# Performance work log

Measured on AMD Instinct MI355X. Metric: run time of the kernel, lower is better.

## Reference

```python
import jax, jax.numpy as jnp
import numpy as np

B, T, N, C = 4, 6, 512, 8
HID, FEAT, EMB, IN_DIM = 64, 16, 32, 1
KS, KC, HORIZON = 3, 2, 3
ALPHA = 3.0

def _init(key, shape):
    fin = shape[-2] if len(shape) >= 2 else shape[-1]
    return jax.random.normal(key, shape, dtype=jnp.float32) * (1.0 / fin) ** 0.5

def setup_inputs():
    ks = jax.random.split(jax.random.key(0), 32)
    L_enc = (IN_DIM + FEAT + HID) * KS * KC
    L_dec = (HID + FEAT + HID) * KS * KC
    return {
        "X_seq": jax.random.normal(ks[0], (B, T, N, C), dtype=jnp.float32),
        "As": jax.random.uniform(ks[1], (N, N), dtype=jnp.float32) / N,
        "Ac": jax.random.uniform(ks[2], (C, C), dtype=jnp.float32) / C,
        "feature": jax.random.normal(ks[3], (N, FEAT), dtype=jnp.float32),
        "Wu_S": _init(ks[4], (C, HID)), "Wv_S": _init(ks[5], (C, HID)),
        "Wu_C": _init(ks[6], (N, HID)), "Wv_C": _init(ks[7], (N, HID)),
        "mfS_w1": _init(ks[8], (4, 2, 256)), "mfS_b1": jnp.zeros((4, 256), jnp.float32),
        "mfS_w2": _init(ks[9], (4, 256, 256)), "mfS_b2": jnp.zeros((4, 256), jnp.float32),
        "mfC_w1": _init(ks[10], (4, 2, 256)), "mfC_b1": jnp.zeros((4, 256), jnp.float32),
        "mfC_w2": _init(ks[11], (4, 256, 256)), "mfC_b2": jnp.zeros((4, 256), jnp.float32),
        "enc_gW": _init(ks[12], (L_enc, 2 * HID)), "enc_gb": jnp.zeros((2 * HID,), jnp.float32),
        "enc_cW": _init(ks[13], (L_enc, HID)), "enc_cb": jnp.zeros((HID,), jnp.float32),
        "dec_gW": _init(ks[14], (L_dec, 2 * HID)), "dec_gb": jnp.zeros((2 * HID,), jnp.float32),
        "dec_cW": _init(ks[15], (L_dec, HID)), "dec_cb": jnp.zeros((HID,), jnp.float32),
        "out_w1": _init(ks[16], (HID, EMB)), "out_b1": jnp.zeros((EMB,), jnp.float32),
        "out_w2": _init(ks[17], (EMB, IN_DIM)), "out_b2": jnp.zeros((IN_DIM,), jnp.float32),
    }

def _mlp(x, w1, b1, w2, b2):
    return jax.nn.relu(x @ w1 + b1) @ w2 + b2

def _mixed_fusion(A, P, w1, b1, w2, b2):
    # node_feat = [rowsum(A), rowsum(P)]; key/value MLPs indexed 0:key_A 1:key_P 2:val_A 3:val_P
    nf = jnp.stack([A.sum(-1), P.sum(-1)], axis=-1)            # [n, 2]
    An, Pn = A @ nf, P @ nf
    key = _mlp(An, w1[0], b1[0], w2[0], b2[0]) + _mlp(Pn, w1[1], b1[1], w2[1], b2[1])
    val = _mlp(An, w1[2], b1[2], w2[2], b2[2]) + _mlp(Pn, w1[3], b1[3], w2[3], b2[3])
    a = jax.nn.sigmoid(key @ val.T)
    return a * A + (1.0 - a) * P

def _adaptive_graph(Xf, Wu, Wv):
    U = jnp.tanh(ALPHA * Xf @ Wu)                              # [b,t,n,h]
    V = jnp.tanh(ALPHA * Xf @ Wv)
    M = jnp.einsum('btnh,btmh->nm', U, V)
    # Ps = softmax(relu(M - M^T)) matches einsum pair in torch source
    return jax.nn.softmax(jax.nn.relu(M - M.T), axis=-1)

def _cheby(G, K):
    mats = [jnp.eye(G.shape[0], dtype=G.dtype), G]
    for _ in range(2, K):
        mats.append(2.0 * G @ mats[-1] - mats[-2])
    return jnp.stack(mats[:K], axis=0)                         # [K, n, n]

def _bdg(X, Gs_set, Gc_set, W, b):
    # X: [b,n,c,l]; fused Ks x Kc Chebyshev mode products; cat order (k, j, l) matches torch cat
    t1 = jnp.einsum('bncl,knm->kbmcl', X, Gs_set)
    t2 = jnp.einsum('kbmcl,jcd->bmdkjl', t1, Gc_set)
    feat = t2.reshape(t2.shape[0], t2.shape[1], t2.shape[2], -1)
    return feat @ W + b

def _cell(Xt, Ht, featx, Gs_set, Gc_set, gW, gb, cW, cb):
    XH = jnp.concatenate([Xt, Ht, featx], axis=-1)
    uv = _bdg(XH, Gs_set, Gc_set, gW, gb)
    update = jax.nn.sigmoid(uv[..., :HID])
    reset = jax.nn.sigmoid(uv[..., HID:])
    cand_in = jnp.concatenate([Xt, reset * Ht, featx], axis=-1)
    cand = jnp.tanh(_bdg(cand_in, Gs_set, Gc_set, cW, cb))
    return (1.0 - update) * Ht + update * cand

def _forward(X_seq, As, Ac, feature, Wu_S, Wv_S, Wu_C, Wv_C,
             mfS_w1, mfS_b1, mfS_w2, mfS_b2, mfC_w1, mfC_b1, mfC_w2, mfC_b2,
             enc_gW, enc_gb, enc_cW, enc_cb, dec_gW, dec_gb, dec_cW, dec_cb,
             out_w1, out_b1, out_w2, out_b2):
    # MGP_Gen: adaptive spatial / categorical graphs fused with priors
    Ps = _adaptive_graph(X_seq, Wu_S, Wv_S)
    Gs = _mixed_fusion(As, Ps, mfS_w1, mfS_b1, mfS_w2, mfS_b2)
    Xc = jnp.swapaxes(X_seq, 2, 3)                             # [b,t,c,n]
    Pc = _adaptive_graph(Xc, Wu_C, Wv_C)
    Gc = _mixed_fusion(Ac, Pc, mfC_w1, mfC_b1, mfC_w2, mfC_b2)
    Gs_set, Gc_set = _cheby(Gs, KS), _cheby(Gc, KC)
    featx = jnp.broadcast_to(feature[None, :, None, :], (B, N, C, FEAT))
    X5 = X_seq[..., None]                                      # [b,t,n,c,1]
    Ht = jnp.zeros((B, N, C, HID), dtype=X_seq.dtype)
    for t in range(T):                                         # encoder GRU over history
        Ht = _cell(X5[:, t], Ht, featx, Gs_set, Gc_set, enc_gW, enc_gb, enc_cW, enc_cb)
    deco_in, Hd = Ht, Ht
    outs = []
    for _ in range(HORIZON):
        Hd = _cell(deco_in, Hd, featx, Gs_set, Gc_set, dec_gW, dec_gb, dec_cW, dec_cb)
        outs.append(_mlp(Hd, out_w1, out_b1, out_w2, out_b2))
        deco_in = Hd
    return jnp.stack(outs, axis=1)                             # [b, horizon, n, c, 1]

def reference(X_seq, As, Ac, feature, Wu_S, Wv_S, Wu_C, Wv_C, mfS_w1, mfS_b1, mfS_w2, mfS_b2, mfC_w1, mfC_b1, mfC_w2, mfC_b2, enc_gW, enc_gb, enc_cW, enc_cb, dec_gW, dec_gb, dec_cW, dec_cb, out_w1, out_b1, out_w2, out_b2):
    return _forward(X_seq, As, Ac, feature, Wu_S, Wv_S, Wu_C, Wv_C, mfS_w1, mfS_b1, mfS_w2, mfS_b2, mfC_w1, mfC_b1, mfC_w2, mfC_b2, enc_gW, enc_gb, enc_cW, enc_cb, dec_gW, dec_gb, dec_cW, dec_cb, out_w1, out_b1, out_w2, out_b2)
```

## Files before the change

### kernel.cpp

```cpp
#include <hip/hip_runtime.h>
#include <math.h>

constexpr int kB = 4, kT = 6, kN = 512, kC = 8;
constexpr int kH = 64, kF = 16, kE = 32;
constexpr int kKS = 3, kKC = 2, kHOR = 3;
constexpr int kBT = kB * kT;
constexpr int kRK = kBT * kH;
constexpr int L_ENC = 1 + kH + kF;
constexpr int L_DEC = kH + kH + kF;
constexpr int PL_ENC = 96;
constexpr int PL_DEC = 160;
constexpr int KP_ENC = 3 * PL_ENC;
constexpr int KP_DGF = 288;
constexpr int KP_DEC = 3 * PL_DEC;
constexpr float kALPHA = 3.0f;

typedef unsigned short ushortT;
typedef short short8 __attribute__((ext_vector_type(8)));
typedef float f32x4 __attribute__((ext_vector_type(4)));

__device__ __forceinline__ float sigm(float x) { return 1.0f / (1.0f + __expf(-x)); }

__device__ __forceinline__ ushortT f2bf(float f) {
    union { float f; unsigned int u; } v; v.f = f;
    unsigned int r = v.u + 0x7fffu + ((v.u >> 16) & 1u);
    return (ushortT)(r >> 16);
}

__device__ __forceinline__ void fma44(const float4& a, const float4& b, float acc[4][4]) {
    acc[0][0] += a.x*b.x; acc[0][1] += a.x*b.y; acc[0][2] += a.x*b.z; acc[0][3] += a.x*b.w;
    acc[1][0] += a.y*b.x; acc[1][1] += a.y*b.y; acc[1][2] += a.y*b.z; acc[1][3] += a.y*b.w;
    acc[2][0] += a.z*b.x; acc[2][1] += a.z*b.y; acc[2][2] += a.z*b.z; acc[2][3] += a.z*b.w;
    acc[3][0] += a.w*b.x; acc[3][1] += a.w*b.y; acc[3][2] += a.w*b.z; acc[3][3] += a.w*b.w;
}


__global__ __launch_bounds__(256) void k_uvproj_s(
    const float* __restrict__ X, const float* __restrict__ Wu, const float* __restrict__ Wv,
    float* __restrict__ Upr, float* __restrict__ Vpr)
{
    int idx = blockIdx.x * blockDim.x + threadIdx.x;
    if (idx >= kN * kBT * kH) return;
    int h = idx % kH; int bt = (idx / kH) % kBT; int n = idx / (kH * kBT);
    const float* xr = X + ((size_t)bt * kN + n) * kC;
    float u = 0.f, v = 0.f;
#pragma unroll
    for (int c = 0; c < kC; ++c) { float x = xr[c]; u += x * Wu[c*kH + h]; v += x * Wv[c*kH + h]; }
    Upr[(size_t)n * kRK + bt * kH + h] = tanhf(kALPHA * u);
    Vpr[(size_t)n * kRK + bt * kH + h] = tanhf(kALPHA * v);
}

__global__ __launch_bounds__(512) void k_uvproj_c2(
    const float* __restrict__ X, const float* __restrict__ WuC, const float* __restrict__ WvC,
    float* __restrict__ Uc, float* __restrict__ Vc)
{
    __shared__ float Xs[4096];
    __shared__ float Wus[4096], Wvs[4096];
    int bt = blockIdx.x, tid = threadIdx.x;
    for (int i = tid; i < 4096; i += 512) Xs[i] = X[(size_t)bt*4096 + i];
    int c = tid >> 6, h = tid & 63;
    float u = 0.f, v = 0.f;
    for (int n0 = 0; n0 < 512; n0 += 64) {
        __syncthreads();
        for (int i = tid; i < 4096; i += 512) { Wus[i] = WuC[n0*64 + i]; Wvs[i] = WvC[n0*64 + i]; }
        __syncthreads();
#pragma unroll 8
        for (int nn = 0; nn < 64; ++nn) {
            float x = Xs[(n0+nn)*8 + c];
            u += x * Wus[nn*64 + h];
            v += x * Wvs[nn*64 + h];
        }
    }
    Uc[(size_t)bt*512 + c*64 + h] = tanhf(kALPHA * u);
    Vc[(size_t)bt*512 + c*64 + h] = tanhf(kALPHA * v);
}

__global__ __launch_bounds__(512) void k_mc2(
    const float* __restrict__ Uc, const float* __restrict__ Vc, float* __restrict__ Mc)
{
    __shared__ float red[512];
    int tid = threadIdx.x;
    int cd = tid & 63, kc = tid >> 6;
    int c = cd >> 3, d = cd & 7;
    float s = 0.f;
    for (int q = kc*192; q < kc*192 + 192; ++q) {
        int bt = q >> 6, h = q & 63;
        s += Uc[(size_t)bt*512 + c*64 + h] * Vc[(size_t)bt*512 + d*64 + h];
    }
    red[tid] = s; __syncthreads();
    for (int st = 256; st >= 64; st >>= 1) { if (tid < st) red[tid] += red[tid + st]; __syncthreads(); }
    if (tid < 64) Mc[tid] = red[tid];
}

__global__ __launch_bounds__(256) void k_nfa(const float* __restrict__ A, float* __restrict__ nf)
{
    int i = blockIdx.x, tid = threadIdx.x;
    __shared__ float sa[256];
    float a = 0.f;
    for (int j = tid; j < kN; j += 256) a += A[(size_t)i*kN + j];
    sa[tid] = a; __syncthreads();
    for (int s = 128; s > 0; s >>= 1) { if (tid < s) sa[tid] += sa[tid+s]; __syncthreads(); }
    if (!tid) { nf[i*2] = sa[0]; nf[i*2+1] = 1.0f; }
}

__global__ __launch_bounds__(256) void k_softmax_anpn(
    const float* __restrict__ M, const float* __restrict__ A, const float* __restrict__ nf,
    float* __restrict__ P, float* __restrict__ An, float* __restrict__ Pn)
{
    int i = blockIdx.x, tid = threadIdx.x;
    __shared__ float s0[256], s1[256], s2[256], s3[256], s4[256];
    float mx = -1e30f;
    for (int j = tid; j < kN; j += 256)
        mx = fmaxf(mx, fmaxf(M[(size_t)i*kN + j] - M[(size_t)j*kN + i], 0.f));
    s0[tid] = mx; __syncthreads();
    for (int s = 128; s > 0; s >>= 1) { if (tid < s) s0[tid] = fmaxf(s0[tid], s0[tid+s]); __syncthreads(); }
    mx = s0[0]; __syncthreads();
    float sum=0, pn0=0, pn1=0, an0=0, an1=0;
    for (int j = tid; j < kN; j += 256) {
        float v = fmaxf(M[(size_t)i*kN + j] - M[(size_t)j*kN + i], 0.f);
        float e = __expf(v - mx);
        P[(size_t)i*kN + j] = e;
        float n0 = nf[2*j], n1 = nf[2*j+1];
        float a = A[(size_t)i*kN + j];
        sum += e; pn0 += e*n0; pn1 += e*n1; an0 += a*n0; an1 += a*n1;
    }
    s0[tid]=sum; s1[tid]=pn0; s2[tid]=pn1; s3[tid]=an0; s4[tid]=an1; __syncthreads();
    for (int s = 128; s > 0; s >>= 1) {
        if (tid < s) { s0[tid]+=s0[tid+s]; s1[tid]+=s1[tid+s]; s2[tid]+=s2[tid+s]; s3[tid]+=s3[tid+s]; s4[tid]+=s4[tid+s]; }
        __syncthreads();
    }
    float inv = 1.f / s0[0];
    if (!tid) { Pn[i*2] = s1[0]*inv; Pn[i*2+1] = s2[0]*inv; An[i*2] = s3[0]; An[i*2+1] = s4[0]; }
    __syncthreads();
    for (int j = tid; j < kN; j += 256) P[(size_t)i*kN + j] *= inv;
}

__global__ __launch_bounds__(256) void k_mlp1cat(
    const float* __restrict__ An, const float* __restrict__ Pn,
    const float* __restrict__ w1, const float* __restrict__ b1, int ia, int ip,
    float* __restrict__ hidAP)
{
    int idx = blockIdx.x * 256 + threadIdx.x;
    if (idx >= 512 * 512) return;
    int col = idx & 511, i = idx >> 9;
    float v;
    if (col < 256) {
        const float* w = w1 + (size_t)ia * 512; const float* b = b1 + (size_t)ia * 256;
        v = An[i*2]*w[col] + An[i*2+1]*w[256 + col] + b[col];
    } else {
        int o = col - 256;
        const float* w = w1 + (size_t)ip * 512; const float* b = b1 + (size_t)ip * 256;
        v = Pn[i*2]*w[o] + Pn[i*2+1]*w[256 + o] + b[o];
    }
    hidAP[idx] = fmaxf(v, 0.f);
}

__global__ __launch_bounds__(256) void k_prep_w2t(
    const float* __restrict__ w2, float* __restrict__ w2tK, float* __restrict__ w2tV)
{
    int idx = blockIdx.x * 256 + threadIdx.x;
    if (idx >= 256 * 512) return;
    int kk = idx & 511, n = idx >> 9;
    int j = kk >> 8, k = kk & 255;
    w2tK[idx] = w2[(size_t)(0 + j)*65536 + k*256 + n];
    w2tV[idx] = w2[(size_t)(2 + j)*65536 + k*256 + n];
}

__global__ __launch_bounds__(256) void k_gemm_ntsk(
    const float* __restrict__ A, const float* __restrict__ B, float* __restrict__ part,
    int M, int N, int K, int skl)
{
    __shared__ __align__(16) float sA[32][68];
    __shared__ __align__(16) float sB[32][68];
    int tid = threadIdx.x, tx = tid & 15, ty = tid >> 4;
    int j0 = blockIdx.x * 64, i0 = blockIdx.y * 64;
    int kb = blockIdx.z * skl;
    float acc[4][4] = {};
    for (int k0 = kb; k0 < kb + skl; k0 += 32) {
#pragma unroll
        for (int it = 0; it < 2; ++it) {
            int q = tid + it * 256;
            int row = q >> 3, ks = (q & 7) * 4;
            float4 va = *(const float4*)&A[(size_t)(i0 + row)*K + k0 + ks];
            float4 vb = *(const float4*)&B[(size_t)(j0 + row)*K + k0 + ks];
            sA[ks+0][row] = va.x; sA[ks+1][row] = va.y; sA[ks+2][row] = va.z; sA[ks+3][row] = va.w;
            sB[ks+0][row] = vb.x; sB[ks+1][row] = vb.y; sB[ks+2][row] = vb.z; sB[ks+3][row] = vb.w;
        }
        __syncthreads();
#pragma unroll
        for (int kk = 0; kk < 32; ++kk) {
            float4 a = *(const float4*)&sA[kk][ty*4];
            float4 b = *(const float4*)&sB[kk][tx*4];
            fma44(a, b, acc);
        }
        __syncthreads();
    }
    float* dst = part + (size_t)blockIdx.z * M * N;
#pragma unroll
    for (int i = 0; i < 4; ++i)
#pragma unroll
        for (int j = 0; j < 4; ++j)
            dst[(size_t)(i0 + ty*4 + i)*N + j0 + tx*4 + j] = acc[i][j];
}

__global__ __launch_bounds__(256) void k_redep(
    const float* __restrict__ part, int SK, int total, int N,
    float* __restrict__ C, int mode,
    const float* __restrict__ p1, const float* __restrict__ p2)
{
    int idx = blockIdx.x * 256 + threadIdx.x;
    if (idx >= total) return;
    float s = 0.f;
    for (int k = 0; k < SK; ++k) s += part[(size_t)k*total + idx];
    if (mode == 1) { float a = sigm(s); s = a*p1[idx] + (1.f - a)*p2[idx]; }
    else if (mode == 2) { int col = idx % N; s += p1[col] + p2[col]; }
    C[idx] = s;
}

__global__ __launch_bounds__(256) void k_catmlp2(
    const float* __restrict__ Mc, const float* __restrict__ Ac,
    const float* __restrict__ w1, const float* __restrict__ b1,
    const float* __restrict__ w2, const float* __restrict__ b2,
    float* __restrict__ keyval)
{
    __shared__ float Pcs[64], rsA[8], Ans[16], Pns[16];
    __shared__ float hA[8][256], hP[8][256];
    int tid = threadIdx.x;
    int kv = blockIdx.x, c0 = blockIdx.y * 64;
    int qa = kv*2, qp = kv*2 + 1;
    if (tid < 8) {
        int i = tid;
        float row[8]; float mx = -1e30f;
#pragma unroll
        for (int j = 0; j < 8; ++j) { float v = fmaxf(Mc[i*8+j] - Mc[j*8+i], 0.f); row[j] = v; mx = fmaxf(mx, v); }
        float s = 0.f;
#pragma unroll
        for (int j = 0; j < 8; ++j) { row[j] = __expf(row[j] - mx); s += row[j]; }
        float inv = 1.f / s;
#pragma unroll
        for (int j = 0; j < 8; ++j) Pcs[i*8+j] = row[j] * inv;
        float a = 0.f;
#pragma unroll
        for (int j = 0; j < 8; ++j) a += Ac[i*8+j];
        rsA[i] = a;
    }
    __syncthreads();
    if (tid < 16) {
        int i = tid >> 1, comp = tid & 1;
        float an = 0.f, pn = 0.f;
#pragma unroll
        for (int j = 0; j < 8; ++j) {
            float nfj = comp ? 1.f : rsA[j];
            an += Ac[i*8+j] * nfj; pn += Pcs[i*8+j] * nfj;
        }
        Ans[i*2+comp] = an; Pns[i*2+comp] = pn;
    }
    __syncthreads();
    for (int e = tid; e < 2048; e += 256) {
        int i = e >> 8, o = e & 255;
        hA[i][o] = fmaxf(Ans[i*2]*w1[qa*512 + o] + Ans[i*2+1]*w1[qa*512 + 256 + o] + b1[qa*256 + o], 0.f);
        hP[i][o] = fmaxf(Pns[i*2]*w1[qp*512 + o] + Pns[i*2+1]*w1[qp*512 + 256 + o] + b1[qp*256 + o], 0.f);
    }
    __syncthreads();
    for (int e = tid; e < 512; e += 256) {
        int i = e >> 6, oc = c0 + (e & 63);
        float s = b2[qa*256 + oc] + b2[qp*256 + oc];
        for (int k = 0; k < 256; ++k)
            s += hA[i][k]*w2[(size_t)qa*65536 + k*256 + oc] + hP[i][k]*w2[(size_t)qp*65536 + k*256 + oc];
        keyval[(size_t)kv*2048 + i*256 + oc] = s;
    }
}

__global__ void k_gcfuse2(const float* __restrict__ keyval, const float* __restrict__ Mc,
                          const float* __restrict__ Ac, float* __restrict__ GcF)
{
    __shared__ float Pcs[64];
    int t = threadIdx.x; if (t >= 64) return;
    if (t < 8) {
        int i = t;
        float row[8]; float mx = -1e30f;
#pragma unroll
        for (int j = 0; j < 8; ++j) { float v = fmaxf(Mc[i*8+j] - Mc[j*8+i], 0.f); row[j] = v; mx = fmaxf(mx, v); }
        float s = 0.f;
#pragma unroll
        for (int j = 0; j < 8; ++j) { row[j] = __expf(row[j] - mx); s += row[j]; }
        float inv = 1.f / s;
#pragma unroll
        for (int j = 0; j < 8; ++j) Pcs[i*8+j] = row[j] * inv;
    }
    __syncthreads();
    int c = t >> 3, d = t & 7;
    const float* key = keyval;
    const float* val = keyval + 2048;
    float s = 0.f;
    for (int k = 0; k < 256; ++k) s += key[c*256 + k] * val[d*256 + k];
    float a = sigm(s);
    GcF[c*8 + d] = a*Ac[c*8 + d] + (1.f - a)*Pcs[c*8 + d];
}


__global__ void k_transp(const float* __restrict__ G, ushortT* __restrict__ Gt)
{
    __shared__ float tile[32][33];
    int bx = blockIdx.x * 32, by = blockIdx.y * 32;
    int x = threadIdx.x, y0 = threadIdx.y;
    for (int yy = y0; yy < 32; yy += 8) tile[yy][x] = G[(size_t)(by+yy)*kN + bx + x];
    __syncthreads();
    for (int yy = y0; yy < 32; yy += 8) Gt[(size_t)(bx+yy)*kN + by + x] = f2bf(tile[x][yy]);
}

__global__ __launch_bounds__(256) void k_prep_wt(
    const float* __restrict__ W, ushortT* __restrict__ WT,
    int L, int PL, int KP, int outW, int mode)
{
    int idx = blockIdx.x * blockDim.x + threadIdx.x;
    if (idx >= 2 * outW * KP) return;
    int qp = idx % KP, o = idx / KP;
    int kk = qp / PL, l = qp - kk * PL;
    int lo;
    if (mode == 1) lo = (l < 64) ? l + 1 : (l == 64) ? 0 : (l < 80) ? L : (l - 15);
    else lo = l;
    int j = o / outW, oo = o - j * outW;
    float v = (lo < L) ? W[(size_t)((kk*2 + j)*L + lo) * outW + oo] : 0.f;
    WT[idx] = f2bf(v);
}

__global__ __launch_bounds__(256) void k_prep_wtgd(
    const float* __restrict__ W, ushortT* __restrict__ WT)
{
    int idx = blockIdx.x * blockDim.x + threadIdx.x;
    if (idx >= 256 * KP_DGF) return;
    int qp = idx % KP_DGF, o = idx / KP_DGF;
    int k = qp / 96, p = qp - k * 96;
    int j = o >> 7, oo = o & 127;
    int base = (k*2 + j) * L_DEC;
    float v;
    if (p < 64)      v = W[(size_t)(base + p)*128 + oo] + W[(size_t)(base + 64 + p)*128 + oo];
    else if (p < 80) v = W[(size_t)(base + 128 + (p - 64))*128 + oo];
    else             v = 0.f;
    WT[idx] = f2bf(v);
}

__global__ __launch_bounds__(256) void k_cheby_mfma(
    const ushortT* __restrict__ Gst, ushortT* __restrict__ Gst2)
{
    __shared__ short sA[128][40];
    __shared__ short sB[128][40];
    int tid = threadIdx.x;
    int m0 = blockIdx.y * 128, j0 = blockIdx.x * 128;
    int w = tid >> 6, lane = tid & 63, wr = w >> 1, wc = w & 1;
    f32x4 acc[4][4];
#pragma unroll
    for (int i = 0; i < 4; ++i)
#pragma unroll
        for (int j = 0; j < 4; ++j) acc[i][j] = (f32x4){0.f, 0.f, 0.f, 0.f};
    for (int k0 = 0; k0 < kN; k0 += 32) {
        {
            int row = tid >> 1, lc = (tid & 1) * 16;
            const ushortT* p = Gst + (size_t)(m0 + row)*kN + k0 + lc;
            *(short8*)&sA[row][lc]     = *(const short8*)p;
            *(short8*)&sA[row][lc + 8] = *(const short8*)(p + 8);
        }
        {
            int kr = tid & 31, jc = (tid >> 5) * 8;
#pragma unroll
            for (int rep = 0; rep < 2; ++rep) {
                short8 v = *(const short8*)(Gst + (size_t)(k0 + kr)*kN + j0 + jc + rep*64);
#pragma unroll
                for (int i = 0; i < 8; ++i) sB[jc + rep*64 + i][kr] = v[i];
            }
        }
        __syncthreads();
        short8 af[4], bfr[4];
#pragma unroll
        for (int mi = 0; mi < 4; ++mi)
            af[mi] = *(const short8*)&sA[wr*64 + mi*16 + (lane & 15)][(lane >> 4) * 8];
#pragma unroll
        for (int ni = 0; ni < 4; ++ni)
            bfr[ni] = *(const short8*)&sB[wc*64 + ni*16 + (lane & 15)][(lane >> 4) * 8];
#pragma unroll
        for (int mi = 0; mi < 4; ++mi)
#pragma unroll
            for (int ni = 0; ni < 4; ++ni)
                acc[mi][ni] = __builtin_amdgcn_mfma_f32_16x16x32_bf16(af[mi], bfr[ni], acc[mi][ni], 0, 0, 0);
        __syncthreads();
    }
#pragma unroll
    for (int mi = 0; mi < 4; ++mi) {
#pragma unroll
        for (int ni = 0; ni < 4; ++ni) {
            int row0 = m0 + wr*64 + mi*16 + (lane >> 4) * 4;
            int col  = j0 + wc*64 + ni*16 + (lane & 15);
#pragma unroll
            for (int q = 0; q < 4; ++q) {
                int row = row0 + q;
                Gst2[(size_t)row*kN + col] = f2bf(2.f*acc[mi][ni][q] - (row == col ? 1.f : 0.f));
            }
        }
    }
}

template<int CLP, int PL, int ACTW, int OFF>
__global__ __launch_bounds__(256) void k_t1m(
    const ushortT* __restrict__ Gst, const ushortT* __restrict__ Xin, ushortT* __restrict__ Yout)
{
    __shared__ short sA[128][40];
    __shared__ short sB[128][40];
    int tid = threadIdx.x;
    int ki = blockIdx.z >> 2, b = blockIdx.z & 3;
    const ushortT* A = Gst + (size_t)ki * kN * kN;
    const ushortT* B = Xin + (size_t)b * kN * CLP;
    ushortT* C = Yout + (size_t)(ki*4 + b) * kN * CLP;
    int m0 = blockIdx.y * 128, j0 = blockIdx.x * 128;
    int w = tid >> 6, lane = tid & 63, wr = w >> 1, wc = w & 1;
    int kr = tid & 31, jc = (tid >> 5) * 8;
    int colr0, colr1;
    { int j = j0 + jc;      int cg = j / ACTW; colr0 = cg*PL + OFF + (j - cg*ACTW); }
    { int j = j0 + jc + 64; int cg = j / ACTW; colr1 = cg*PL + OFF + (j - cg*ACTW); }
    f32x4 acc[4][4];
#pragma unroll
    for (int i = 0; i < 4; ++i)
#pragma unroll
        for (int j = 0; j < 4; ++j) acc[i][j] = (f32x4){0.f, 0.f, 0.f, 0.f};

    for (int k0 = 0; k0 < kN; k0 += 32) {
        {
            int row = tid >> 1, lc = (tid & 1) * 16;
            const ushortT* p = A + (size_t)(m0 + row)*kN + k0 + lc;
            *(short8*)&sA[row][lc]     = *(const short8*)p;
            *(short8*)&sA[row][lc + 8] = *(const short8*)(p + 8);
        }
        {
            short8 v0 = *(const short8*)(B + (size_t)(k0 + kr)*CLP + colr0);
            short8 v1 = *(const short8*)(B + (size_t)(k0 + kr)*CLP + colr1);
#pragma unroll
            for (int i = 0; i < 8; ++i) sB[jc + i][kr] = v0[i];
#pragma unroll
            for (int i = 0; i < 8; ++i) sB[jc + 64 + i][kr] = v1[i];
        }
        __syncthreads();
        short8 af[4], bfr[4];
#pragma unroll
        for (int mi = 0; mi < 4; ++mi)
            af[mi] = *(const short8*)&sA[wr*64 + mi*16 + (lane & 15)][(lane >> 4) * 8];
#pragma unroll
        for (int ni = 0; ni < 4; ++ni)
            bfr[ni] = *(const short8*)&sB[wc*64 + ni*16 + (lane & 15)][(lane >> 4) * 8];
#pragma unroll
        for (int mi = 0; mi < 4; ++mi)
#pragma unroll
            for (int ni = 0; ni < 4; ++ni)
                acc[mi][ni] = __builtin_amdgcn_mfma_f32_16x16x32_bf16(af[mi], bfr[ni], acc[mi][ni], 0, 0, 0);
        __syncthreads();
    }
#pragma unroll
    for (int mi = 0; mi < 4; ++mi) {
#pragma unroll
        for (int ni = 0; ni < 4; ++ni) {
            int row = m0 + wr*64 + mi*16 + (lane >> 4) * 4;
            int fj = j0 + wc*64 + ni*16;
            int cg = fj / ACTW;
            int col = cg*PL + OFF + (fj - cg*ACTW) + (lane & 15);
#pragma unroll
            for (int q = 0; q < 4; ++q)
                C[(size_t)(row + q)*CLP + col] = f2bf(acc[mi][ni][q]);
        }
    }
}

template<int PL, int NQ, int MODE, int FN>
__global__ __launch_bounds__(256) void k_gg(
    const ushortT* __restrict__ XH, const ushortT* __restrict__ Yb,
    const ushortT* __restrict__ WT, float* __restrict__ Cout)
{
    constexpr int BN = 32 * FN;
    constexpr int KP = NQ * 32;
    constexpr int Ntot = 64 * FN;
    __shared__ short sA[128][40];
    __shared__ short sB[BN][40];
    int tid = threadIdx.x;
    int r0 = blockIdx.y * 128, j0 = blockIdx.x * BN;
    int b = r0 >> 12, rr = r0 & 4095;
    const ushortT* src0 = XH + (size_t)r0 * PL;
    const ushortT* src1 = Yb + ((size_t)b       * 4096 + rr) * PL;
    const ushortT* src2 = Yb + ((size_t)(4 + b) * 4096 + rr) * PL;
    int w = tid >> 6, lane = tid & 63, wr = w >> 1, wc = w & 1;
    f32x4 acc[4][FN];
#pragma unroll
    for (int i = 0; i < 4; ++i)
#pragma unroll
        for (int j = 0; j < FN; ++j) acc[i][j] = (f32x4){0.f, 0.f, 0.f, 0.f};

    for (int q = 0; q < NQ; ++q) {
        int k, off;
        if (MODE == 0)      { k = q/3; off = (q - k*3)*32; }
        else if (MODE == 1) { k = q/3; int part = q - k*3; off = (part < 2) ? part*32 : 128; }
        else                { k = q/5; off = (q - k*5)*32; }
        const ushortT* Ap = (k == 0) ? src0 : (k == 1) ? src1 : src2;
        {
            int row = tid >> 1, lc = (tid & 1) * 16;
            const ushortT* p = Ap + (size_t)row * PL + off + lc;
            *(short8*)&sA[row][lc]     = *(const short8*)p;
            *(short8*)&sA[row][lc + 8] = *(const short8*)(p + 8);
        }
        if (FN == 4) {
            int col = tid >> 1, seg = (tid & 1) * 16;
            const ushortT* p = WT + (size_t)(j0 + col)*KP + q*32 + seg;
            *(short8*)&sB[col][seg]     = *(const short8*)p;
            *(short8*)&sB[col][seg + 8] = *(const short8*)(p + 8);
        } else {
            int col = tid >> 2, seg = (tid & 3) * 8;
            *(short8*)&sB[col][seg] = *(const short8*)(WT + (size_t)(j0 + col)*KP + q*32 + seg);
        }
        __syncthreads();
        short8 af[4], bfr[FN];
#pragma unroll
        for (int mi = 0; mi < 4; ++mi)
            af[mi] = *(const short8*)&sA[wr*64 + mi*16 + (lane & 15)][(lane >> 4) * 8];
#pragma unroll
        for (int ni = 0; ni < FN; ++ni)
            bfr[ni] = *(const short8*)&sB[wc*16*FN + ni*16 + (lane & 15)][(lane >> 4) * 8];
#pragma unroll
        for (int mi = 0; mi < 4; ++mi)
#pragma unroll
            for (int ni = 0; ni < FN; ++ni)
                acc[mi][ni] = __builtin_amdgcn_mfma_f32_16x16x32_bf16(af[mi], bfr[ni], acc[mi][ni], 0, 0, 0);
        __syncthreads();
    }
#pragma unroll
    for (int mi = 0; mi < 4; ++mi) {
#pragma unroll
        for (int ni = 0; ni < FN; ++ni) {
            int row = r0 + wr*64 + mi*16 + (lane >> 4) * 4;
            int col = j0 + wc*16*FN + ni*16 + (lane & 15);
#pragma unroll
            for (int q = 0; q < 4; ++q)
                Cout[(size_t)(row + q)*Ntot + col] = acc[mi][ni][q];
        }
    }
}


template<int PL, int XOFF>
__global__ __launch_bounds__(256) void k_gates_ep(
    const float* __restrict__ Gg, const float* __restrict__ GcM,
    const float* __restrict__ gb, const float* __restrict__ Ht,
    float* __restrict__ upd, ushortT* __restrict__ XH)
{
    __shared__ float sG[8][256];
    __shared__ float GcS[64];
    int tid = threadIdx.x, bm = blockIdx.x;
    const float* src = Gg + (size_t)bm * 2048;
    for (int i = tid; i < 2048; i += 256) sG[i >> 8][i & 255] = src[i];
    if (tid < 64) GcS[tid] = GcM[tid];
    __syncthreads();
    int d = tid >> 5, o0 = (tid & 31) * 4;
    size_t rb = (size_t)bm * 8 + d;
#pragma unroll
    for (int q = 0; q < 4; ++q) {
        int o = o0 + q;
        float pre = sG[d][o] + gb[o];
#pragma unroll
        for (int c = 0; c < 8; ++c) pre += GcS[c*8 + d] * sG[c][128 + o];
        float g = sigm(pre);
        if (o < kH) upd[rb*kH + o] = g;
        else {
            int h = o - kH;
            XH[rb*PL + XOFF + h] = f2bf(g * Ht[rb*kH + h]);
        }
    }
}

template<int MODE>
__global__ __launch_bounds__(256) void k_cand_ep(
    const float* __restrict__ Gc2, const float* __restrict__ GcM,
    const float* __restrict__ cb, const float* __restrict__ upd,
    float* __restrict__ Ht, ushortT* __restrict__ XHo,
    const float* __restrict__ X, int tnext,
    const float* __restrict__ ow1, const float* __restrict__ ob1,
    const float* __restrict__ ow2, const float* __restrict__ ob2,
    float* __restrict__ out, int hz)
{
    __shared__ float sG[8][128];
    __shared__ float GcS[64];
    __shared__ float Hn[8][65];
    __shared__ float Pp[8][32];
    int tid = threadIdx.x, bm = blockIdx.x;
    const float* src = Gc2 + (size_t)bm * 1024;
    for (int i = tid; i < 1024; i += 256) sG[i >> 7][i & 127] = src[i];
    if (tid < 64) GcS[tid] = GcM[tid];
    __syncthreads();
    int d = tid >> 5, o0 = (tid & 31) * 2;
    size_t rb = (size_t)bm * 8 + d;
#pragma unroll
    for (int jj = 0; jj < 2; ++jj) {
        int o = o0 + jj;
        float pre = sG[d][o] + cb[o];
#pragma unroll
        for (int c = 0; c < 8; ++c) pre += GcS[c*8 + d] * sG[c][64 + o];
        float cv = tanhf(pre);
        float u = upd[rb*kH + o];
        float h0 = Ht[rb*kH + o];
        float hn = (1.f - u)*h0 + u*cv;
        Ht[rb*kH + o] = hn;
        if (MODE >= 2) Hn[d][o] = hn;
        if (MODE == 0)      XHo[rb*PL_ENC + o] = f2bf(hn);
        else if (MODE <= 2) XHo[rb*PL_DEC + o] = f2bf(hn);
    }
    if (MODE == 0) {
        if (tid < 8) {
            int r = bm*8 + tid;
            int c2 = r & 7, m = (r >> 3) & 511, b2 = r >> 12;
            XHo[(size_t)r*PL_ENC + 64] = f2bf(X[(((size_t)b2*kT + tnext)*kN + m)*kC + c2]);
        }
    }
    if (MODE >= 2) {
        __syncthreads();
        int row = tid >> 5, e = tid & 31;
        float s = ob1[e];
#pragma unroll
        for (int k = 0; k < kH; ++k) s += Hn[row][k] * ow1[k*kE + e];
        Pp[row][e] = fmaxf(s, 0.f) * ow2[e];
        __syncthreads();
        if (tid < 8) {
            float v = ob2[0];
#pragma unroll
            for (int e2 = 0; e2 < 32; ++e2) v += Pp[tid][e2];
            int r = bm*8 + tid;
            int c2 = r & 7, m = (r >> 3) & 511, b2 = r >> 12;
            out[((size_t)(b2*kHOR + hz)*kN + m)*kC + c2] = v;
        }
    }
}

__global__ __launch_bounds__(256) void k_build_enc0(
    const float* __restrict__ X, const float* __restrict__ featr, ushortT* __restrict__ XH)
{
    int idx = blockIdx.x * blockDim.x + threadIdx.x;
    if (idx >= 16384 * PL_ENC) return;
    int l = idx % PL_ENC; int r = idx / PL_ENC;
    float v;
    if (l < 64)       v = 0.f;
    else if (l == 64) { int c = r & 7, m = (r >> 3) & 511, b = r >> 12; v = X[(((size_t)b*kT)*kN + m)*kC + c]; }
    else if (l < 80)  v = 0.f;
    else              { int m = (r >> 3) & 511; v = featr[m*kF + (l - 80)]; }
    XH[idx] = f2bf(v);
}

__global__ __launch_bounds__(256) void k_initdec(
    const float* __restrict__ featr, ushortT* __restrict__ XHd)
{
    int idx = blockIdx.x * blockDim.x + threadIdx.x;
    if (idx >= 16384 * 32) return;
    int l2 = idx & 31; int r = idx >> 5;
    float v = (l2 < 16) ? featr[((r >> 3) & 511)*kF + l2] : 0.f;
    XHd[(size_t)r*PL_DEC + 128 + l2] = f2bf(v);
}

extern "C" void kernel_launch(void* const* d_in, const int* in_sizes, int n_in,
                              void* d_out, int out_size, void* d_ws, size_t ws_size,
                              hipStream_t stream)
{
    (void)in_sizes; (void)n_in; (void)out_size; (void)ws_size;
    const float* X      = (const float*)d_in[0];
    const float* As     = (const float*)d_in[1];
    const float* Ac     = (const float*)d_in[2];
    const float* featr  = (const float*)d_in[3];
    const float* WuS    = (const float*)d_in[4];
    const float* WvS    = (const float*)d_in[5];
    const float* WuC    = (const float*)d_in[6];
    const float* WvC    = (const float*)d_in[7];
    const float* mfS_w1 = (const float*)d_in[8];
    const float* mfS_b1 = (const float*)d_in[9];
    const float* mfS_w2 = (const float*)d_in[10];
    const float* mfS_b2 = (const float*)d_in[11];
    const float* mfC_w1 = (const float*)d_in[12];
    const float* mfC_b1 = (const float*)d_in[13];
    const float* mfC_w2 = (const float*)d_in[14];
    const float* mfC_b2 = (const float*)d_in[15];
    const float* enc_gW = (const float*)d_in[16];
    const float* enc_gb = (const float*)d_in[17];
    const float* enc_cW = (const float*)d_in[18];
    const float* enc_cb = (const float*)d_in[19];
    const float* dec_gW = (const float*)d_in[20];
    const float* dec_gb = (const float*)d_in[21];
    const float* dec_cW = (const float*)d_in[22];
    const float* dec_cb = (const float*)d_in[23];
    const float* out_w1 = (const float*)d_in[24];
    const float* out_b1 = (const float*)d_in[25];
    const float* out_w2 = (const float*)d_in[26];
    const float* out_b2 = (const float*)d_in[27];
    float* out = (float*)d_out;
    float* ws = (float*)d_ws;

    float* Ht     = ws;
    float* updb   = Ht + 1048576;
    float* Gg     = updb + 1048576;
    float* Gs     = Gg + 4194304;
    float* smallf = Gs + 262144;
    float* nfS = smallf;
    float* AnS = nfS + 1024;
    float* PnS = AnS + 1024;
    float* McB = PnS + 1024;
    float* GcF = McB + 64;
    float* kvC = GcF + 64;
    ushortT* XHb  = (ushortT*)(smallf + 8192);
    ushortT* Yb   = XHb + 2621440;
    ushortT* GstB = Yb + 5242880;
    ushortT* WTg_e = GstB + 524288;
    ushortT* WTc_e = WTg_e + 73728;
    ushortT* WTg_d = WTc_e + 36864;
    ushortT* WTc_d = WTg_d + 122880;
    ushortT* XHd   = WTc_d + 61440;
    float* Upr   = Gg;
    float* Vpr   = Upr + 786432;
    float* part  = Vpr + 786432;
    float* Ms    = part + 1048576;
    float* Ps    = Ms + 262144;
    float* hidAP = Ps + 262144;
    float* keyS  = hidAP + 262144;
    float* valS  = keyS + 131072;
    float* w2tK  = valS + 131072;
    float* w2tV  = w2tK + 131072;
    float* Uc    = w2tV + 131072;
    float* Vc    = Uc + 12288;

    constexpr int CLP_ENC = kC * PL_ENC;
    constexpr int CLP_DEC = kC * PL_DEC;

    hipMemsetAsync(Ht, 0, (size_t)16384 * kH * sizeof(float), stream);

    k_prep_wt<<<(2*128*KP_ENC + 255)/256, 256, 0, stream>>>(enc_gW, WTg_e, L_ENC, PL_ENC, KP_ENC, 128, 1);
    k_prep_wt<<<(2*64 *KP_ENC + 255)/256, 256, 0, stream>>>(enc_cW, WTc_e, L_ENC, PL_ENC, KP_ENC, 64, 1);
    k_prep_wtgd<<<(256*KP_DGF + 255)/256, 256, 0, stream>>>(dec_gW, WTg_d);
    k_prep_wt<<<(2*64 *KP_DEC + 255)/256, 256, 0, stream>>>(dec_cW, WTc_d, L_DEC, PL_DEC, KP_DEC, 64, 0);
    k_prep_w2t<<<512, 256, 0, stream>>>(mfS_w2, w2tK, w2tV);

    k_uvproj_s<<<(kN*kBT*kH + 255)/256, 256, 0, stream>>>(X, WuS, WvS, Upr, Vpr);
    k_gemm_ntsk<<<dim3(8, 8, 4), 256, 0, stream>>>(Upr, Vpr, part, 512, 512, 1536, 384);
    k_redep<<<1024, 256, 0, stream>>>(part, 4, 262144, 512, Ms, 0, nullptr, nullptr);
    k_nfa<<<kN, 256, 0, stream>>>(As, nfS);
    k_softmax_anpn<<<kN, 256, 0, stream>>>(Ms, As, nfS, Ps, AnS, PnS);
    k_mlp1cat<<<1024, 256, 0, stream>>>(AnS, PnS, mfS_w1, mfS_b1, 0, 1, hidAP);
    k_gemm_ntsk<<<dim3(4, 8, 2), 256, 0, stream>>>(hidAP, w2tK, part, 512, 256, 512, 256);
    k_redep<<<512, 256, 0, stream>>>(part, 2, 131072, 256, keyS, 2, mfS_b2, mfS_b2 + 256);
    k_mlp1cat<<<1024, 256, 0, stream>>>(AnS, PnS, mfS_w1, mfS_b1, 2, 3, hidAP);
    k_gemm_ntsk<<<dim3(4, 8, 2), 256, 0, stream>>>(hidAP, w2tV, part, 512, 256, 512, 256);
    k_redep<<<512, 256, 0, stream>>>(part, 2, 131072, 256, valS, 2, mfS_b2 + 512, mfS_b2 + 768);
    k_gemm_ntsk<<<dim3(8, 8, 2), 256, 0, stream>>>(keyS, valS, part, 512, 512, 256, 128);
    k_redep<<<1024, 256, 0, stream>>>(part, 2, 262144, 512, Gs, 1, As, Ps);
    k_transp<<<dim3(16, 16), dim3(32, 8), 0, stream>>>(Gs, GstB);
    k_cheby_mfma<<<dim3(4, 4), 256, 0, stream>>>(GstB, GstB + 262144);

    k_uvproj_c2<<<kBT, 512, 0, stream>>>(X, WuC, WvC, Uc, Vc);
    k_mc2<<<1, 512, 0, stream>>>(Uc, Vc, McB);
    k_catmlp2<<<dim3(2, 4), 256, 0, stream>>>(McB, Ac, mfC_w1, mfC_b1, mfC_w2, mfC_b2, kvC);
    k_gcfuse2<<<1, 64, 0, stream>>>(kvC, McB, Ac, GcF);

    k_build_enc0<<<(16384*PL_ENC + 255)/256, 256, 0, stream>>>(X, featr, XHb);
    k_initdec<<<(16384*32 + 255)/256, 256, 0, stream>>>(featr, XHd);

    k_t1m<CLP_ENC, PL_ENC, 16, 80><<<dim3(1, 4, 8), 256, 0, stream>>>(GstB, XHb, Yb);
    for (int t = 0; t < kT; ++t) {
        k_t1m<CLP_ENC, PL_ENC, 80, 0><<<dim3(5, 4, 8), 256, 0, stream>>>(GstB, XHb, Yb);
        k_gg<PL_ENC, 9, 0, 4><<<dim3(2, 128), 256, 0, stream>>>(XHb, Yb, WTg_e, Gg);
        k_gates_ep<PL_ENC, 0><<<2048, 256, 0, stream>>>(Gg, GcF, enc_gb, Ht, updb, XHb);
        k_t1m<CLP_ENC, PL_ENC, 64, 0><<<dim3(4, 4, 8), 256, 0, stream>>>(GstB, XHb, Yb);
        k_gg<PL_ENC, 9, 0, 2><<<dim3(2, 128), 256, 0, stream>>>(XHb, Yb, WTc_e, Gg);
        if (t < kT - 1)
            k_cand_ep<0><<<2048, 256, 0, stream>>>(Gg, GcF, enc_cb, updb, Ht, XHb, X, t + 1,
                                                   nullptr, nullptr, nullptr, nullptr, nullptr, 0);
        else
            k_cand_ep<1><<<2048, 256, 0, stream>>>(Gg, GcF, enc_cb, updb, Ht, XHd, nullptr, 0,
                                                   nullptr, nullptr, nullptr, nullptr, nullptr, 0);
    }

    k_t1m<CLP_DEC, PL_DEC, 16, 128><<<dim3(1, 4, 8), 256, 0, stream>>>(GstB, XHd, Yb);
    for (int hz = 0; hz < kHOR; ++hz) {
        k_t1m<CLP_DEC, PL_DEC, 64, 0><<<dim3(4, 4, 8), 256, 0, stream>>>(GstB, XHd, Yb);
        k_gg<PL_DEC, 9, 1, 4><<<dim3(2, 128), 256, 0, stream>>>(XHd, Yb, WTg_d, Gg);
        k_gates_ep<PL_DEC, 64><<<2048, 256, 0, stream>>>(Gg, GcF, dec_gb, Ht, updb, XHd);
        k_t1m<CLP_DEC, PL_DEC, 64, 64><<<dim3(4, 4, 8), 256, 0, stream>>>(GstB, XHd, Yb);
        k_gg<PL_DEC, 15, 2, 2><<<dim3(2, 128), 256, 0, stream>>>(XHd, Yb, WTc_d, Gg);
        if (hz < kHOR - 1)
            k_cand_ep<2><<<2048, 256, 0, stream>>>(Gg, GcF, dec_cb, updb, Ht, XHd, nullptr, 0,
                                                   out_w1, out_b1, out_w2, out_b2, out, hz);
        else
            k_cand_ep<3><<<2048, 256, 0, stream>>>(Gg, GcF, dec_cb, updb, Ht, XHd, nullptr, 0,
                                                   out_w1, out_b1, out_w2, out_b2, out, hz);
    }
}
```

Measured before the change: 973.1 us.

## Fuse setup kernels to cut launches and intermediate buffers

After: 963.7 us. No clear change (-1.0%).

```diff
diff --git a/kernel.cpp b/kernel.cpp
--- a/kernel.cpp
+++ b/kernel.cpp
@@ -34,13 +34,74 @@
     acc[3][0] += a.w*b.x; acc[3][1] += a.w*b.y; acc[3][2] += a.w*b.z; acc[3][3] += a.w*b.w;
 }
 
-
-__global__ __launch_bounds__(256) void k_uvproj_s(
+__global__ __launch_bounds__(256) void k_prep_all(
+    const float* __restrict__ egW, const float* __restrict__ ecW,
+    const float* __restrict__ dgW, const float* __restrict__ dcW,
+    const float* __restrict__ w2,
+    ushortT* __restrict__ WTg_e, ushortT* __restrict__ WTc_e,
+    ushortT* __restrict__ WTg_d, ushortT* __restrict__ WTc_d,
+    float* __restrict__ w2tK, float* __restrict__ w2tV)
+{
+    int idx = blockIdx.x * 256 + threadIdx.x;
+    if (idx < 73728) {
+        int qp = idx % KP_ENC, o = idx / KP_ENC;
+        int kk = qp / PL_ENC, l = qp - kk * PL_ENC;
+        int lo = (l < 64) ? l + 1 : (l == 64) ? 0 : (l < 80) ? L_ENC : (l - 15);
+        int j = o / 128, oo = o - j * 128;
+        float v = (lo < L_ENC) ? egW[(size_t)((kk*2 + j)*L_ENC + lo) * 128 + oo] : 0.f;
+        WTg_e[idx] = f2bf(v);
+    } else if (idx < 110592) {
+        int r = idx - 73728;
+        int qp = r % KP_ENC, o = r / KP_ENC;
+        int kk = qp / PL_ENC, l = qp - kk * PL_ENC;
+        int lo = (l < 64) ? l + 1 : (l == 64) ? 0 : (l < 80) ? L_ENC : (l - 15);
+        int j = o / 64, oo = o - j * 64;
+        float v = (lo < L_ENC) ? ecW[(size_t)((kk*2 + j)*L_ENC + lo) * 64 + oo] : 0.f;
+        WTc_e[r] = f2bf(v);
+    } else if (idx < 184320) {
+        int r = idx - 110592;
+        int qp = r % KP_DGF, o = r / KP_DGF;
+        int k = qp / 96, p = qp - k * 96;
+        int j = o >> 7, oo = o & 127;
+        int base = (k*2 + j) * L_DEC;
+        float v;
+        if (p < 64)      v = dgW[(size_t)(base + p)*128 + oo] + dgW[(size_t)(base + 64 + p)*128 + oo];
+        else if (p < 80) v = dgW[(size_t)(base + 128 + (p - 64))*128 + oo];
+        else             v = 0.f;
+        WTg_d[r] = f2bf(v);
+    } else if (idx < 245760) {
+        int r = idx - 184320;
+        int qp = r % KP_DEC, o = r / KP_DEC;
+        int kk = qp / PL_DEC, l = qp - kk * PL_DEC;
+        int j = o / 64, oo = o - j * 64;
+        float v = (l < L_DEC) ? dcW[(size_t)((kk*2 + j)*L_DEC + l) * 64 + oo] : 0.f;
+        WTc_d[r] = f2bf(v);
+    } else if (idx < 376832) {
+        int r = idx - 245760;
+        int kk = r & 511, n = r >> 9;
+        int j = kk >> 8, k = kk & 255;
+        w2tK[r] = w2[(size_t)(0 + j)*65536 + k*256 + n];
+        w2tV[r] = w2[(size_t)(2 + j)*65536 + k*256 + n];
+    }
+}
+
+
+__global__ __launch_bounds__(256) void k_uvproj_s_nfa(
     const float* __restrict__ X, const float* __restrict__ Wu, const float* __restrict__ Wv,
-    float* __restrict__ Upr, float* __restrict__ Vpr)
-{
-    int idx = blockIdx.x * blockDim.x + threadIdx.x;
-    if (idx >= kN * kBT * kH) return;
+    const float* __restrict__ As,
+    float* __restrict__ Upr, float* __restrict__ Vpr, float* __restrict__ nf)
+{
+    if (blockIdx.x >= 3072) {
+        int i = blockIdx.x - 3072, tid = threadIdx.x;
+        __shared__ float sa[256];
+        float a = 0.f;
+        for (int j = tid; j < kN; j += 256) a += As[(size_t)i*kN + j];
+        sa[tid] = a; __syncthreads();
+        for (int s = 128; s > 0; s >>= 1) { if (tid < s) sa[tid] += sa[tid+s]; __syncthreads(); }
+        if (!tid) { nf[i*2] = sa[0]; nf[i*2+1] = 1.0f; }
+        return;
+    }
+    int idx = blockIdx.x * 256 + threadIdx.x;
     int h = idx % kH; int bt = (idx / kH) % kBT; int n = idx / (kH * kBT);
     const float* xr = X + ((size_t)bt * kN + n) * kC;
     float u = 0.f, v = 0.f;
@@ -75,49 +136,25 @@
     Vc[(size_t)bt*512 + c*64 + h] = tanhf(kALPHA * v);
 }
 
-__global__ __launch_bounds__(512) void k_mc2(
-    const float* __restrict__ Uc, const float* __restrict__ Vc, float* __restrict__ Mc)
-{
-    __shared__ float red[512];
-    int tid = threadIdx.x;
-    int cd = tid & 63, kc = tid >> 6;
-    int c = cd >> 3, d = cd & 7;
-    float s = 0.f;
-    for (int q = kc*192; q < kc*192 + 192; ++q) {
-        int bt = q >> 6, h = q & 63;
-        s += Uc[(size_t)bt*512 + c*64 + h] * Vc[(size_t)bt*512 + d*64 + h];
-    }
-    red[tid] = s; __syncthreads();
-    for (int st = 256; st >= 64; st >>= 1) { if (tid < st) red[tid] += red[tid + st]; __syncthreads(); }
-    if (tid < 64) Mc[tid] = red[tid];
-}
-
-__global__ __launch_bounds__(256) void k_nfa(const float* __restrict__ A, float* __restrict__ nf)
-{
-    int i = blockIdx.x, tid = threadIdx.x;
-    __shared__ float sa[256];
-    float a = 0.f;
-    for (int j = tid; j < kN; j += 256) a += A[(size_t)i*kN + j];
-    sa[tid] = a; __syncthreads();
-    for (int s = 128; s > 0; s >>= 1) { if (tid < s) sa[tid] += sa[tid+s]; __syncthreads(); }
-    if (!tid) { nf[i*2] = sa[0]; nf[i*2+1] = 1.0f; }
-}
-
 __global__ __launch_bounds__(256) void k_softmax_anpn(
-    const float* __restrict__ M, const float* __restrict__ A, const float* __restrict__ nf,
+    const float* __restrict__ part, const float* __restrict__ A, const float* __restrict__ nf,
     float* __restrict__ P, float* __restrict__ An, float* __restrict__ Pn)
 {
     int i = blockIdx.x, tid = threadIdx.x;
     __shared__ float s0[256], s1[256], s2[256], s3[256], s4[256];
+    auto mval = [&](int r, int c2) -> float {
+        size_t id = (size_t)r*kN + c2;
+        return part[id] + part[262144 + id] + part[524288 + id] + part[786432 + id];
+    };
     float mx = -1e30f;
     for (int j = tid; j < kN; j += 256)
-        mx = fmaxf(mx, fmaxf(M[(size_t)i*kN + j] - M[(size_t)j*kN + i], 0.f));
+        mx = fmaxf(mx, fmaxf(mval(i, j) - mval(j, i), 0.f));
     s0[tid] = mx; __syncthreads();
     for (int s = 128; s > 0; s >>= 1) { if (tid < s) s0[tid] = fmaxf(s0[tid], s0[tid+s]); __syncthreads(); }
     mx = s0[0]; __syncthreads();
     float sum=0, pn0=0, pn1=0, an0=0, an1=0;
     for (int j = tid; j < kN; j += 256) {
-        float v = fmaxf(M[(size_t)i*kN + j] - M[(size_t)j*kN + i], 0.f);
+        float v = fmaxf(mval(i, j) - mval(j, i), 0.f);
         float e = __expf(v - mx);
         P[(size_t)i*kN + j] = e;
         float n0 = nf[2*j], n1 = nf[2*j+1];
@@ -135,35 +172,26 @@
     for (int j = tid; j < kN; j += 256) P[(size_t)i*kN + j] *= inv;
 }
 
-__global__ __launch_bounds__(256) void k_mlp1cat(
+__global__ __launch_bounds__(256) void k_mlp1kv(
     const float* __restrict__ An, const float* __restrict__ Pn,
-    const float* __restrict__ w1, const float* __restrict__ b1, int ia, int ip,
-    float* __restrict__ hidAP)
+    const float* __restrict__ w1, const float* __restrict__ b1, float* __restrict__ hid)
 {
     int idx = blockIdx.x * 256 + threadIdx.x;
-    if (idx >= 512 * 512) return;
-    int col = idx & 511, i = idx >> 9;
+    if (idx >= 524288) return;
+    int half = idx >> 18;
+    int r = idx & 262143;
+    int col = r & 511, i = r >> 9;
+    int ia = half*2, ip = half*2 + 1;
     float v;
     if (col < 256) {
-        const float* w = w1 + (size_t)ia * 512; const float* b = b1 + (size_t)ia * 256;
-        v = An[i*2]*w[col] + An[i*2+1]*w[256 + col] + b[col];
+        const float* w = w1 + (size_t)ia * 512;
+        v = An[i*2]*w[col] + An[i*2+1]*w[256 + col] + b1[ia*256 + col];
     } else {
         int o = col - 256;
-        const float* w = w1 + (size_t)ip * 512; const float* b = b1 + (size_t)ip * 256;
-        v = Pn[i*2]*w[o] + Pn[i*2+1]*w[256 + o] + b[o];
-    }
-    hidAP[idx] = fmaxf(v, 0.f);
-}
-
-__global__ __launch_bounds__(256) void k_prep_w2t(
-    const float* __restrict__ w2, float* __restrict__ w2tK, float* __restrict__ w2tV)
-{
-    int idx = blockIdx.x * 256 + threadIdx.x;
-    if (idx >= 256 * 512) return;
-    int kk = idx & 511, n = idx >> 9;
-    int j = kk >> 8, k = kk & 255;
-    w2tK[idx] = w2[(size_t)(0 + j)*65536 + k*256 + n];
-    w2tV[idx] = w2[(size_t)(2 + j)*65536 + k*256 + n];
+        const float* w = w1 + (size_t)ip * 512;
+        v = Pn[i*2]*w[o] + Pn[i*2+1]*w[256 + o] + b1[ip*256 + o];
+    }
+    hid[idx] = fmaxf(v, 0.f);
 }
 
 __global__ __launch_bounds__(256) void k_gemm_ntsk(
@@ -203,36 +231,145 @@
             dst[(size_t)(i0 + ty*4 + i)*N + j0 + tx*4 + j] = acc[i][j];
 }
 
-__global__ __launch_bounds__(256) void k_redep(
-    const float* __restrict__ part, int SK, int total, int N,
-    float* __restrict__ C, int mode,
-    const float* __restrict__ p1, const float* __restrict__ p2)
+__global__ __launch_bounds__(256) void k_ntsk_kv(
+    const float* __restrict__ hid, const float* __restrict__ w2t, float* __restrict__ part)
+{
+    __shared__ __align__(16) float sA[32][68];
+    __shared__ __align__(16) float sB[32][68];
+    int tid = threadIdx.x, tx = tid & 15, ty = tid >> 4;
+    int z = blockIdx.z;
+    const float* A = hid + (size_t)(z >> 1) * 262144;
+    const float* B = w2t + (size_t)(z >> 1) * 131072;
+    int kb = (z & 1) * 256;
+    int j0 = blockIdx.x * 64, i0 = blockIdx.y * 64;
+    float acc[4][4] = {};
+    for (int k0 = kb; k0 < kb + 256; k0 += 32) {
+#pragma unroll
+        for (int it = 0; it < 2; ++it) {
+            int q = tid + it * 256;
+            int row = q >> 3, ks = (q & 7) * 4;
+            float4 va = *(const float4*)&A[(size_t)(i0 + row)*512 + k0 + ks];
+            float4 vb = *(const float4*)&B[(size_t)(j0 + row)*512 + k0 + ks];
+            sA[ks+0][row] = va.x; sA[ks+1][row] = va.y; sA[ks+2][row] = va.z; sA[ks+3][row] = va.w;
+            sB[ks+0][row] = vb.x; sB[ks+1][row] = vb.y; sB[ks+2][row] = vb.z; sB[ks+3][row] = vb.w;
+        }
+        __syncthreads();
+#pragma unroll
+        for (int kk = 0; kk < 32; ++kk) {
+            float4 a = *(const float4*)&sA[kk][ty*4];
+            float4 b = *(const float4*)&sB[kk][tx*4];
+            fma44(a, b, acc);
+        }
+        __syncthreads();
+    }
+    float* dst = part + (size_t)z * 131072;
+#pragma unroll
+    for (int i = 0; i < 4; ++i)
+#pragma unroll
+        for (int j = 0; j < 4; ++j)
+            dst[(size_t)(i0 + ty*4 + i)*256 + j0 + tx*4 + j] = acc[i][j];
+}
+
+__global__ __launch_bounds__(256) void k_redep_kv(
+    const float* __restrict__ part, const float* __restrict__ b2, float* __restrict__ keyval)
 {
     int idx = blockIdx.x * 256 + threadIdx.x;
-    if (idx >= total) return;
-    float s = 0.f;
-    for (int k = 0; k < SK; ++k) s += part[(size_t)k*total + idx];
-    if (mode == 1) { float a = sigm(s); s = a*p1[idx] + (1.f - a)*p2[idx]; }
-    else if (mode == 2) { int col = idx % N; s += p1[col] + p2[col]; }
-    C[idx] = s;
-}
-
-__global__ __launch_bounds__(256) void k_catmlp2(
-    const float* __restrict__ Mc, const float* __restrict__ Ac,
+    if (idx >= 262144) return;
+    int half = idx >> 17, off = idx & 131071, col = idx & 255;
+    float s = part[(size_t)(half*2)*131072 + off] + part[(size_t)(half*2 + 1)*131072 + off];
+    s += b2[half*512 + col] + b2[half*512 + 256 + col];
+    keyval[idx] = s;
+}
+
+__global__ void k_fuse_transp(
+    const float* __restrict__ part, const float* __restrict__ As,
+    const float* __restrict__ Ps, ushortT* __restrict__ Gt)
+{
+    __shared__ float tile[32][33];
+    int bx = blockIdx.x * 32, by = blockIdx.y * 32;
+    int x = threadIdx.x, y0 = threadIdx.y;
+    for (int yy = y0; yy < 32; yy += 8) {
+        size_t id = (size_t)(by + yy)*kN + bx + x;
+        float s = part[id] + part[262144 + id];
+        float a = sigm(s);
+        tile[yy][x] = a*As[id] + (1.f - a)*Ps[id];
+    }
+    __syncthreads();
+    for (int yy = y0; yy < 32; yy += 8) Gt[(size_t)(bx+yy)*kN + by + x] = f2bf(tile[x][yy]);
+}
+
+__global__ __launch_bounds__(256) void k_cheby64(
+    const ushortT* __restrict__ Gst, ushortT* __restrict__ Gst2)
+{
+    __shared__ short sA[64][40];
+    __shared__ short sB[64][40];
+    int tid = threadIdx.x;
+    int m0 = blockIdx.y * 64, j0 = blockIdx.x * 64;
+    int w = tid >> 6, lane = tid & 63;
+    f32x4 acc[4];
+#pragma unroll
+    for (int i = 0; i < 4; ++i) acc[i] = (f32x4){0.f, 0.f, 0.f, 0.f};
+    for (int k0 = 0; k0 < kN; k0 += 32) {
+        {
+            int row = tid >> 2, lc = (tid & 3) * 8;
+            *(short8*)&sA[row][lc] = *(const short8*)(Gst + (size_t)(m0 + row)*kN + k0 + lc);
+        }
+        {
+            int kr = tid & 31, jc = (tid >> 5) * 8;
+            short8 v = *(const short8*)(Gst + (size_t)(k0 + kr)*kN + j0 + jc);
+#pragma unroll
+            for (int i = 0; i < 8; ++i) sB[jc + i][kr] = v[i];
+        }
+        __syncthreads();
+        short8 bf = *(const short8*)&sB[w*16 + (lane & 15)][(lane >> 4) * 8];
+#pragma unroll
+        for (int mi = 0; mi < 4; ++mi) {
+            short8 af = *(const short8*)&sA[mi*16 + (lane & 15)][(lane >> 4) * 8];
+            acc[mi] = __builtin_amdgcn_mfma_f32_16x16x32_bf16(af, bf, acc[mi], 0, 0, 0);
+        }
+        __syncthreads();
+    }
+#pragma unroll
+    for (int mi = 0; mi < 4; ++mi) {
+        int row0 = m0 + mi*16 + (lane >> 4)*4;
+        int col = j0 + w*16 + (lane & 15);
+#pragma unroll
+        for (int q = 0; q < 4; ++q) {
+            int row = row0 + q;
+            Gst2[(size_t)row*kN + col] = f2bf(2.f*acc[mi][q] - (row == col ? 1.f : 0.f));
+        }
+    }
+}
+
+__global__ __launch_bounds__(512) void k_catall(
+    const float* __restrict__ Uc, const float* __restrict__ Vc, const float* __restrict__ Ac,
     const float* __restrict__ w1, const float* __restrict__ b1,
     const float* __restrict__ w2, const float* __restrict__ b2,
-    float* __restrict__ keyval)
-{
-    __shared__ float Pcs[64], rsA[8], Ans[16], Pns[16];
-    __shared__ float hA[8][256], hP[8][256];
+    float* __restrict__ GcF)
+{
+    __shared__ float red[512];
+    __shared__ float McS[64], Pcs[64], rsA[8], Ans[16], Pns[16];
+    __shared__ float hA[2][8][256], hP[2][8][256];
+    __shared__ float kv[2][8][256];
     int tid = threadIdx.x;
-    int kv = blockIdx.x, c0 = blockIdx.y * 64;
-    int qa = kv*2, qp = kv*2 + 1;
+    {
+        int cd = tid & 63, kc = tid >> 6;
+        int c = cd >> 3, d = cd & 7;
+        float s = 0.f;
+        for (int q = kc*192; q < kc*192 + 192; ++q) {
+            int bt = q >> 6, h = q & 63;
+            s += Uc[(size_t)bt*512 + c*64 + h] * Vc[(size_t)bt*512 + d*64 + h];
+        }
+        red[tid] = s; __syncthreads();
+        for (int st = 256; st >= 64; st >>= 1) { if (tid < st) red[tid] += red[tid + st]; __syncthreads(); }
+        if (tid < 64) McS[tid] = red[tid];
+    }
+    __syncthreads();
     if (tid < 8) {
         int i = tid;
         float row[8]; float mx = -1e30f;
 #pragma unroll
-        for (int j = 0; j < 8; ++j) { float v = fmaxf(Mc[i*8+j] - Mc[j*8+i], 0.f); row[j] = v; mx = fmaxf(mx, v); }
+        for (int j = 0; j < 8; ++j) { float v = fmaxf(McS[i*8+j] - McS[j*8+i], 0.f); row[j] = v; mx = fmaxf(mx, v); }
         float s = 0.f;
 #pragma unroll
         for (int j = 0; j < 8; ++j) { row[j] = __expf(row[j] - mx); s += row[j]; }
@@ -256,147 +393,28 @@
         Ans[i*2+comp] = an; Pns[i*2+comp] = pn;
     }
     __syncthreads();
-    for (int e = tid; e < 2048; e += 256) {
-        int i = e >> 8, o = e & 255;
-        hA[i][o] = fmaxf(Ans[i*2]*w1[qa*512 + o] + Ans[i*2+1]*w1[qa*512 + 256 + o] + b1[qa*256 + o], 0.f);
-        hP[i][o] = fmaxf(Pns[i*2]*w1[qp*512 + o] + Pns[i*2+1]*w1[qp*512 + 256 + o] + b1[qp*256 + o], 0.f);
-    }
-    __syncthreads();
-    for (int e = tid; e < 512; e += 256) {
-        int i = e >> 6, oc = c0 + (e & 63);
+    for (int e = tid; e < 4096; e += 512) {
+        int kvi = e >> 11, r = e & 2047; int i = r >> 8, o = r & 255;
+        int qa = kvi*2, qp = kvi*2 + 1;
+        hA[kvi][i][o] = fmaxf(Ans[i*2]*w1[qa*512 + o] + Ans[i*2+1]*w1[qa*512 + 256 + o] + b1[qa*256 + o], 0.f);
+        hP[kvi][i][o] = fmaxf(Pns[i*2]*w1[qp*512 + o] + Pns[i*2+1]*w1[qp*512 + 256 + o] + b1[qp*256 + o], 0.f);
+    }
+    __syncthreads();
+    for (int e = tid; e < 4096; e += 512) {
+        int kvi = e >> 11, r = e & 2047; int i = r >> 8, oc = r & 255;
+        int qa = kvi*2, qp = kvi*2 + 1;
         float s = b2[qa*256 + oc] + b2[qp*256 + oc];
         for (int k = 0; k < 256; ++k)
-            s += hA[i][k]*w2[(size_t)qa*65536 + k*256 + oc] + hP[i][k]*w2[(size_t)qp*65536 + k*256 + oc];
-        keyval[(size_t)kv*2048 + i*256 + oc] = s;
-    }
-}
-
-__global__ void k_gcfuse2(const float* __restrict__ keyval, const float* __restrict__ Mc,
-                          const float* __restrict__ Ac, float* __restrict__ GcF)
-{
-    __shared__ float Pcs[64];
-    int t = threadIdx.x; if (t >= 64) return;
-    if (t < 8) {
-        int i = t;
-        float row[8]; float mx = -1e30f;
-#pragma unroll
-        for (int j = 0; j < 8; ++j) { float v = fmaxf(Mc[i*8+j] - Mc[j*8+i], 0.f); row[j] = v; mx = fmaxf(mx, v); }
+            s += hA[kvi][i][k]*w2[(size_t)qa*65536 + k*256 + oc] + hP[kvi][i][k]*w2[(size_t)qp*65536 + k*256 + oc];
+        kv[kvi][i][oc] = s;
+    }
+    __syncthreads();
+    if (tid < 64) {
+        int c = tid >> 3, d = tid & 7;
         float s = 0.f;
-#pragma unroll
-        for (int j = 0; j < 8; ++j) { row[j] = __expf(row[j] - mx); s += row[j]; }
-        float inv = 1.f / s;
-#pragma unroll
-        for (int j = 0; j < 8; ++j) Pcs[i*8+j] = row[j] * inv;
-    }
-    __syncthreads();
-    int c = t >> 3, d = t & 7;
-    const float* key = keyval;
-    const float* val = keyval + 2048;
-    float s = 0.f;
-    for (int k = 0; k < 256; ++k) s += key[c*256 + k] * val[d*256 + k];
-    float a = sigm(s);
-    GcF[c*8 + d] = a*Ac[c*8 + d] + (1.f - a)*Pcs[c*8 + d];
-}
-
-
-__global__ void k_transp(const float* __restrict__ G, ushortT* __restrict__ Gt)
-{
-    __shared__ float tile[32][33];
-    int bx = blockIdx.x * 32, by = blockIdx.y * 32;
-    int x = threadIdx.x, y0 = threadIdx.y;
-    for (int yy = y0; yy < 32; yy += 8) tile[yy][x] = G[(size_t)(by+yy)*kN + bx + x];
-    __syncthreads();
-    for (int yy = y0; yy < 32; yy += 8) Gt[(size_t)(bx+yy)*kN + by + x] = f2bf(tile[x][yy]);
-}
-
-__global__ __launch_bounds__(256) void k_prep_wt(
-    const float* __restrict__ W, ushortT* __restrict__ WT,
-    int L, int PL, int KP, int outW, int mode)
-{
-    int idx = blockIdx.x * blockDim.x + threadIdx.x;
-    if (idx >= 2 * outW * KP) return;
-    int qp = idx % KP, o = idx / KP;
-    int kk = qp / PL, l = qp - kk * PL;
-    int lo;
-    if (mode == 1) lo = (l < 64) ? l + 1 : (l == 64) ? 0 : (l < 80) ? L : (l - 15);
-    else lo = l;
-    int j = o / outW, oo = o - j * outW;
-    float v = (lo < L) ? W[(size_t)((kk*2 + j)*L + lo) * outW + oo] : 0.f;
-    WT[idx] = f2bf(v);
-}
-
-__global__ __launch_bounds__(256) void k_prep_wtgd(
-    const float* __restrict__ W, ushortT* __restrict__ WT)
-{
-    int idx = blockIdx.x * blockDim.x + threadIdx.x;
-    if (idx >= 256 * KP_DGF) return;
-    int qp = idx % KP_DGF, o = idx / KP_DGF;
-    int k = qp / 96, p = qp - k * 96;
-    int j = o >> 7, oo = o & 127;
-    int base = (k*2 + j) * L_DEC;
-    float v;
-    if (p < 64)      v = W[(size_t)(base + p)*128 + oo] + W[(size_t)(base + 64 + p)*128 + oo];
-    else if (p < 80) v = W[(size_t)(base + 128 + (p - 64))*128 + oo];
-    else             v = 0.f;
-    WT[idx] = f2bf(v);
-}
-
-__global__ __launch_bounds__(256) void k_cheby_mfma(
-    const ushortT* __restrict__ Gst, ushortT* __restrict__ Gst2)
-{
-    __shared__ short sA[128][40];
-    __shared__ short sB[128][40];
-    int tid = threadIdx.x;
-    int m0 = blockIdx.y * 128, j0 = blockIdx.x * 128;
-    int w = tid >> 6, lane = tid & 63, wr = w >> 1, wc = w & 1;
-    f32x4 acc[4][4];
-#pragma unroll
-    for (int i = 0; i < 4; ++i)
-#pragma unroll
-        for (int j = 0; j < 4; ++j) acc[i][j] = (f32x4){0.f, 0.f, 0.f, 0.f};
-    for (int k0 = 0; k0 < kN; k0 += 32) {
-        {
-            int row = tid >> 1, lc = (tid & 1) * 16;
-            const ushortT* p = Gst + (size_t)(m0 + row)*kN + k0 + lc;
-            *(short8*)&sA[row][lc]     = *(const short8*)p;
-            *(short8*)&sA[row][lc + 8] = *(const short8*)(p + 8);
-        }
-        {
-            int kr = tid & 31, jc = (tid >> 5) * 8;
-#pragma unroll
-            for (int rep = 0; rep < 2; ++rep) {
-                short8 v = *(const short8*)(Gst + (size_t)(k0 + kr)*kN + j0 + jc + rep*64);
-#pragma unroll
-                for (int i = 0; i < 8; ++i) sB[jc + rep*64 + i][kr] = v[i];
-            }
-        }
-        __syncthreads();
-        short8 af[4], bfr[4];
-#pragma unroll
-        for (int mi = 0; mi < 4; ++mi)
-            af[mi] = *(const short8*)&sA[wr*64 + mi*16 + (lane & 15)][(lane >> 4) * 8];
-#pragma unroll
-        for (int ni = 0; ni < 4; ++ni)
-            bfr[ni] = *(const short8*)&sB[wc*64 + ni*16 + (lane & 15)][(lane >> 4) * 8];
-#pragma unroll
-        for (int mi = 0; mi < 4; ++mi)
-#pragma unroll
-            for (int ni = 0; ni < 4; ++ni)
-                acc[mi][ni] = __builtin_amdgcn_mfma_f32_16x16x32_bf16(af[mi], bfr[ni], acc[mi][ni], 0, 0, 0);
-        __syncthreads();
-    }
-#pragma unroll
-    for (int mi = 0; mi < 4; ++mi) {
-#pragma unroll
-        for (int ni = 0; ni < 4; ++ni) {
-            int row0 = m0 + wr*64 + mi*16 + (lane >> 4) * 4;
-            int col  = j0 + wc*64 + ni*16 + (lane & 15);
-#pragma unroll
-            for (int q = 0; q < 4; ++q) {
-                int row = row0 + q;
-                Gst2[(size_t)row*kN + col] = f2bf(2.f*acc[mi][ni][q] - (row == col ? 1.f : 0.f));
-            }
-        }
+        for (int k = 0; k < 256; ++k) s += kv[0][c][k] * kv[1][d][k];
+        float a = sigm(s);
+        GcF[tid] = a*Ac[tid] + (1.f - a)*Pcs[tid];
     }
 }
 
@@ -633,28 +651,27 @@
     }
 }
 
-__global__ __launch_bounds__(256) void k_build_enc0(
-    const float* __restrict__ X, const float* __restrict__ featr, ushortT* __restrict__ XH)
-{
-    int idx = blockIdx.x * blockDim.x + threadIdx.x;
-    if (idx >= 16384 * PL_ENC) return;
-    int l = idx % PL_ENC; int r = idx / PL_ENC;
-    float v;
-    if (l < 64)       v = 0.f;
-    else if (l == 64) { int c = r & 7, m = (r >> 3) & 511, b = r >> 12; v = X[(((size_t)b*kT)*kN + m)*kC + c]; }
-    else if (l < 80)  v = 0.f;
-    else              { int m = (r >> 3) & 511; v = featr[m*kF + (l - 80)]; }
-    XH[idx] = f2bf(v);
-}
-
-__global__ __launch_bounds__(256) void k_initdec(
-    const float* __restrict__ featr, ushortT* __restrict__ XHd)
-{
-    int idx = blockIdx.x * blockDim.x + threadIdx.x;
-    if (idx >= 16384 * 32) return;
-    int l2 = idx & 31; int r = idx >> 5;
-    float v = (l2 < 16) ? featr[((r >> 3) & 511)*kF + l2] : 0.f;
-    XHd[(size_t)r*PL_DEC + 128 + l2] = f2bf(v);
+__global__ __launch_bounds__(256) void k_build_init(
+    const float* __restrict__ X, const float* __restrict__ featr,
+    ushortT* __restrict__ XHe, ushortT* __restrict__ XHd, float* __restrict__ Ht)
+{
+    int idx = blockIdx.x * 256 + threadIdx.x;
+    if (idx < 1572864) {
+        int l = idx % PL_ENC; int r = idx / PL_ENC;
+        float v;
+        if (l < 64)       v = 0.f;
+        else if (l == 64) { int c = r & 7, m = (r >> 3) & 511, b = r >> 12; v = X[(((size_t)b*kT)*kN + m)*kC + c]; }
+        else if (l < 80)  v = 0.f;
+        else              { int m = (r >> 3) & 511; v = featr[m*kF + (l - 80)]; }
+        XHe[idx] = f2bf(v);
+    } else if (idx < 2097152) {
+        int r2 = idx - 1572864;
+        int l2 = r2 & 31; int r = r2 >> 5;
+        float v = (l2 < 16) ? featr[((r >> 3) & 511)*kF + l2] : 0.f;
+        XHd[(size_t)r*PL_DEC + 128 + l2] = f2bf(v);
+    } else if (idx < 3145728) {
+        Ht[idx - 2097152] = 0.f;
+    }
 }
 
 extern "C" void kernel_launch(void* const* d_in, const int* in_sizes, int n_in,
@@ -696,14 +713,12 @@
     float* Ht     = ws;
     float* updb   = Ht + 1048576;
     float* Gg     = updb + 1048576;
-    float* Gs     = Gg + 4194304;
-    float* smallf = Gs + 262144;
+    float* Gs_pad = Gg + 4194304;
+    float* smallf = Gs_pad + 262144;
     float* nfS = smallf;
     float* AnS = nfS + 1024;
     float* PnS = AnS + 1024;
-    float* McB = PnS + 1024;
-    float* GcF = McB + 64;
-    float* kvC = GcF + 64;
+    float* GcF = PnS + 1024;
     ushortT* XHb  = (ushortT*)(smallf + 8192);
     ushortT* Yb   = XHb + 2621440;
     ushortT* GstB = Yb + 5242880;
@@ -715,54 +730,40 @@
     float* Upr   = Gg;
     float* Vpr   = Upr + 786432;
     float* part  = Vpr + 786432;
-    float* Ms    = part + 1048576;
-    float* Ps    = Ms + 262144;
-    float* hidAP = Ps + 262144;
-    float* keyS  = hidAP + 262144;
-    float* valS  = keyS + 131072;
-    float* w2tK  = valS + 131072;
-    float* w2tV  = w2tK + 131072;
-    float* Uc    = w2tV + 131072;
+    float* Ps    = part + 1048576;
+    float* hidKV = Ps + 262144;
+    float* keyval= hidKV + 524288;
+    float* w2tKV = keyval + 262144;
+    float* Uc    = updb;
     float* Vc    = Uc + 12288;
 
     constexpr int CLP_ENC = kC * PL_ENC;
     constexpr int CLP_DEC = kC * PL_DEC;
 
-    hipMemsetAsync(Ht, 0, (size_t)16384 * kH * sizeof(float), stream);
-
-    k_prep_wt<<<(2*128*KP_ENC + 255)/256, 256, 0, stream>>>(enc_gW, WTg_e, L_ENC, PL_ENC, KP_ENC, 128, 1);
-    k_prep_wt<<<(2*64 *KP_ENC + 255)/256, 256, 0, stream>>>(enc_cW, WTc_e, L_ENC, PL_ENC, KP_ENC, 64, 1);
-    k_prep_wtgd<<<(256*KP_DGF + 255)/256, 256, 0, stream>>>(dec_gW, WTg_d);
-    k_prep_wt<<<(2*64 *KP_DEC + 255)/256, 256, 0, stream>>>(dec_cW, WTc_d, L_DEC, PL_DEC, KP_DEC, 64, 0);
-    k_prep_w2t<<<512, 256, 0, stream>>>(mfS_w2, w2tK, w2tV);
-
-    k_uvproj_s<<<(kN*kBT*kH + 255)/256, 256, 0, stream>>>(X, WuS, WvS, Upr, Vpr);
+    k_prep_all<<<1472, 256, 0, stream>>>(enc_gW, enc_cW, dec_gW, dec_cW, mfS_w2,
+                                         WTg_e, WTc_e, WTg_d, WTc_d,
+                                         w2tKV, w2tKV + 131072);
+
+    k_uvproj_s_nfa<<<3584, 256, 0, stream>>>(X, WuS, WvS, As, Upr, Vpr, nfS);
     k_gemm_ntsk<<<dim3(8, 8, 4), 256, 0, stream>>>(Upr, Vpr, part, 512, 512, 1536, 384);
-    k_redep<<<1024, 256, 0, stream>>>(part, 4, 262144, 512, Ms, 0, nullptr, nullptr);
-    k_nfa<<<kN, 256, 0, stream>>>(As, nfS);
-    k_softmax_anpn<<<kN, 256, 0, stream>>>(Ms, As, nfS, Ps, AnS, PnS);
-    k_mlp1cat<<<1024, 256, 0, stream>>>(AnS, PnS, mfS_w1, mfS_b1, 0, 1, hidAP);
-    k_gemm_ntsk<<<dim3(4, 8, 2), 256, 0, stream>>>(hidAP, w2tK, part, 512, 256, 512, 256);
-    k_redep<<<512, 256, 0, stream>>>(part, 2, 131072, 256, keyS, 2, mfS_b2, mfS_b2 + 256);
-    k_mlp1cat<<<1024, 256, 0, stream>>>(AnS, PnS, mfS_w1, mfS_b1, 2, 3, hidAP);
-    k_gemm_ntsk<<<dim3(4, 8, 2), 256, 0, stream>>>(hidAP, w2tV, part, 512, 256, 512, 256);
-    k_redep<<<512, 256, 0, stream>>>(part, 2, 131072, 256, valS, 2, mfS_b2 + 512, mfS_b2 + 768);
-    k_gemm_ntsk<<<dim3(8, 8, 2), 256, 0, stream>>>(keyS, valS, part, 512, 512, 256, 128);
-    k_redep<<<1024, 256, 0, stream>>>(part, 2, 262144, 512, Gs, 1, As, Ps);
-    k_transp<<<dim3(16, 16), dim3(32, 8), 0, stream>>>(Gs, GstB);
-    k_cheby_mfma<<<dim3(4, 4), 256, 0, stream>>>(GstB, GstB + 262144);
+    k_softmax_anpn<<<kN, 256, 0, stream>>>(part, As, nfS, Ps, AnS, PnS);
+    k_mlp1kv<<<2048, 256, 0, stream>>>(AnS, PnS, mfS_w1, mfS_b1, hidKV);
+    k_ntsk_kv<<<dim3(4, 8, 4), 256, 0, stream>>>(hidKV, w2tKV, part);
+    k_redep_kv<<<1024, 256, 0, stream>>>(part, mfS_b2, keyval);
+    k_gemm_ntsk<<<dim3(8, 8, 2), 256, 0, stream>>>(keyval, keyval + 131072, part, 512, 512, 256, 128);
+    k_fuse_transp<<<dim3(16, 16), dim3(32, 8), 0, stream>>>(part, As, Ps, GstB);
+    k_cheby64<<<dim3(8, 8), 256, 0, stream>>>(GstB, GstB + 262144);
 
     k_uvproj_c2<<<kBT, 512, 0, stream>>>(X, WuC, WvC, Uc, Vc);
-    k_mc2<<<1, 512, 0, stream>>>(Uc, Vc, McB);
-    k_catmlp2<<<dim3(2, 4), 256, 0, stream>>>(McB, Ac, mfC_w1, mfC_b1, mfC_w2, mfC_b2, kvC);
-    k_gcfuse2<<<1, 64, 0, stream>>>(kvC, McB, Ac, GcF);
-
-    k_build_enc0<<<(16384*PL_ENC + 255)/256, 256, 0, stream>>>(X, featr, XHb);
-    k_initdec<<<(16384*32 + 255)/256, 256, 0, stream>>>(featr, XHd);
-
-    k_t1m<CLP_ENC, PL_ENC, 16, 80><<<dim3(1, 4, 8), 256, 0, stream>>>(GstB, XHb, Yb);
+    k_catall<<<1, 512, 0, stream>>>(Uc, Vc, Ac, mfC_w1, mfC_b1, mfC_w2, mfC_b2, GcF);
+
+    k_build_init<<<12288, 256, 0, stream>>>(X, featr, XHb, XHd, Ht);
+
     for (int t = 0; t < kT; ++t) {
-        k_t1m<CLP_ENC, PL_ENC, 80, 0><<<dim3(5, 4, 8), 256, 0, stream>>>(GstB, XHb, Yb);
+        if (t == 0)
+            k_t1m<CLP_ENC, PL_ENC, 96, 0><<<dim3(6, 4, 8), 256, 0, stream>>>(GstB, XHb, Yb);
+        else
+            k_t1m<CLP_ENC, PL_ENC, 80, 0><<<dim3(5, 4, 8), 256, 0, stream>>>(GstB, XHb, Yb);
         k_gg<PL_ENC, 9, 0, 4><<<dim3(2, 128), 256, 0, stream>>>(XHb, Yb, WTg_e, Gg);
         k_gates_ep<PL_ENC, 0><<<2048, 256, 0, stream>>>(Gg, GcF, enc_gb, Ht, updb, XHb);
         k_t1m<CLP_ENC, PL_ENC, 64, 0><<<dim3(4, 4, 8), 256, 0, stream>>>(GstB, XHb, Yb);
```
